# Performance work log

Hardware: AMD Instinct MI355X
Metric: run time of the kernel (lower is better)

The kernel has to match this reference:

```python
import jax, jax.numpy as jnp
import numpy as np

B, N, E, D, L = 64, 128, 2048, 128, 4  # graphs, nodes/graph, edges/graph, channels, gnn layers
T = B * N  # total batched nodes


def setup_inputs() -> dict:
    key = jax.random.key(0)
    ks = jax.random.split(key, 16)
    s = 1.0 / np.sqrt(D)
    sc = 1.0 / np.sqrt(2 * D)
    inp = {
        "x": jax.random.normal(ks[0], (B, N, D), jnp.float32),
        "edges": jax.random.randint(ks[1], (B, 2, E), 0, N, dtype=jnp.int32),
        "Wg": jax.random.normal(ks[2], (L, D, D), jnp.float32) * s,
        "bg": jnp.zeros((L, D), jnp.float32),
        "Wq": jax.random.normal(ks[3], (D, D), jnp.float32) * s,
        "bq": jnp.zeros((D,), jnp.float32),
        "Wk": jax.random.normal(ks[4], (D, D), jnp.float32) * s,
        "bk": jnp.zeros((D,), jnp.float32),
        "Wv": jax.random.normal(ks[5], (D, D), jnp.float32) * s,
        "bv": jnp.zeros((D,), jnp.float32),
        "Wo": jax.random.normal(ks[6], (D, D), jnp.float32) * s,
        "bo": jnp.zeros((D,), jnp.float32),
        "Wc": jax.random.normal(ks[7], (2 * D, D), jnp.float32) * sc,
        "bc": jnp.zeros((D,), jnp.float32),
    }
    return inp


def _batched_edges(edges):
    # offset per-graph edge indices into the flat [T] node space, add self-loops
    off = (jnp.arange(B, dtype=edges.dtype) * N)[:, None]
    src = (edges[:, 0, :] + off).reshape(-1)
    dst = (edges[:, 1, :] + off).reshape(-1)
    loops = jnp.arange(T, dtype=edges.dtype)
    src = jnp.concatenate([src, loops])
    dst = jnp.concatenate([dst, loops])
    return src, dst


def reference(x, edges, Wg, bg, Wq, bq, Wk, bk, Wv, bv, Wo, bo, Wc, bc):
    xf = x.reshape(T, D)  # flat batched node features (torch_geo_batch.x)
    src, dst = _batched_edges(edges)
    # GCN symmetric normalization with self-loops: deg >= 1
    deg = jax.ops.segment_sum(jnp.ones(src.shape, xf.dtype), dst, num_segments=T)
    norm = jax.lax.rsqrt(deg)
    coef = (norm[src] * norm[dst])[:, None]
    # n_layers of GCNConv + tanh
    h = xf
    for l in range(L):
        m = h @ Wg[l]  # [T, D]
        h = jax.ops.segment_sum(m[src] * coef, dst, num_segments=T) + bg[l]
        h = jnp.tanh(h)
    batch_embedding = h.reshape(B, N, D)
    # DoubleHeadedAttention on the ORIGINAL batched input x; both inputs are
    # identical so the two attention heads compute the same tensor.
    q = xf @ Wq + bq
    k = xf @ Wk + bk
    v = xf @ Wv + bv
    attn = jax.nn.softmax(q @ k.T, axis=-1)  # [T, T]
    attended = (attn @ v) @ Wo + bo  # output_layer, == attended_input1 == attended_input2
    combined = jnp.concatenate([attended, attended], axis=-1)  # [T, 2D]
    att_output = combined @ Wc + bc  # combination_layer
    return jnp.concatenate([batch_embedding, att_output.reshape(B, N, D)], axis=-1)
```

## Files before the change

kernel.cpp:

```cpp
#include <hip/hip_runtime.h>
#include <math.h>

#define TT 8192
#define DD 128
#define GB 64
#define GN 128
#define GE 2048

#define WS_W2      (644u<<10)
#define WS_B2      (708u<<10)
#define WS_Q16     (1u<<20)
#define WS_K16     (3u<<20)
#define WS_VT      (5u<<20)
#define WS_OPART   (7u<<20)
#define WS_PM      (23u<<20)
#define WS_PL      ((23u<<20)+(256u<<10))

typedef _Float16 hfrag  __attribute__((ext_vector_type(8)));
typedef _Float16 h4     __attribute__((ext_vector_type(4)));
typedef float    ffrag  __attribute__((ext_vector_type(4)));

#define MFMA16(a,b,c) __builtin_amdgcn_mfma_f32_16x16x32_f16((a),(b),(c),0,0,0)

typedef __attribute__((address_space(1))) unsigned int gu32_t;
typedef __attribute__((address_space(3))) unsigned int lu32_t;
#define GLOAD16(gp, lp) __builtin_amdgcn_global_load_lds((gu32_t*)(const void*)(gp), (lu32_t*)(void*)(lp), 16, 0, 0)

__device__ __forceinline__ int fidx(int r_, int c_) {
  return (((r_>>4)*4 + (c_>>5))*64 + (r_&15) + 16*((c_>>3)&3))*8 + (c_&7);
}

__device__ __forceinline__ float tanh_fast(float x) {
  float e = __expf(2.f*x);
  return 1.f - 2.f/(e+1.f);
}

__global__ __launch_bounds__(512,1) void fused_pre(
    const float* __restrict__ x, const int* __restrict__ edges,
    const float* __restrict__ Wg, const float* __restrict__ bg,
    const float* __restrict__ Wq, const float* __restrict__ bq_,
    const float* __restrict__ Wk, const float* __restrict__ bk_,
    const float* __restrict__ Wv, const float* __restrict__ bv_,
    const float* __restrict__ Wo, const float* __restrict__ bo,
    const float* __restrict__ Wc, const float* __restrict__ bc,
    _Float16* __restrict__ q16, _Float16* __restrict__ k16, _Float16* __restrict__ vT,
    float* __restrict__ W2, float* __restrict__ b2,
    float* __restrict__ out)
{
  __shared__ __align__(16) char Lm[135168];
  const int tid  = threadIdx.x;
  const int bid  = blockIdx.x;

  if (bid < 64) {
    float*    Af  = (float*)Lm;
    _Float16* W16 = (_Float16*)Lm;
    _Float16* m16 = (_Float16*)(Lm + 32768);
    _Float16* h16 = (_Float16*)(Lm + 65536);
    _Float16* A16 = (_Float16*)(Lm + 98304);
    int*      cnt = (int*)(Lm + 131072);
    float*    nrm = (float*)(Lm + 131584);

    const int lane = tid & 63;
    const int w8   = tid >> 6;
    const int l15  = lane & 15;
    const int g    = lane >> 4;
    const int wi   = w8 >> 2;
    const int wj   = w8 & 3;
    const int b    = bid;
    const int* eg  = edges + b*2*GE;

    #pragma unroll
    for (int i=0;i<8;++i) ((float4*)Af)[i*512 + tid] = (float4){0.f,0.f,0.f,0.f};
    if (tid < 128) cnt[tid] = 0;
    __syncthreads();
    #pragma unroll
    for (int i=0;i<4;++i) atomicAdd(&cnt[eg[GE + i*512 + tid]], 1);
    __syncthreads();
    if (tid < 128) nrm[tid] = rsqrtf(1.f + (float)cnt[tid]);
    __syncthreads();
    #pragma unroll
    for (int i=0;i<4;++i){
      int s = eg[i*512 + tid], d = eg[GE + i*512 + tid];
      atomicAdd(&Af[d*128 + s], nrm[s]*nrm[d]);
    }
    __syncthreads();
    if (tid < 128) Af[tid*128 + tid] += nrm[tid]*nrm[tid];
    __syncthreads();
    #pragma unroll
    for (int i=0;i<8;++i){
      int i4 = i*512 + tid;
      float4 v = ((const float4*)Af)[i4];
      int dst = i4>>5, s4 = (i4&31)<<2;
      h4 t; t[0]=(_Float16)v.x; t[1]=(_Float16)v.y; t[2]=(_Float16)v.z; t[3]=(_Float16)v.w;
      *(h4*)&A16[fidx(dst, s4)] = t;
    }
    #pragma unroll
    for (int i=0;i<8;++i){
      int i4 = i*512 + tid;
      int n = i4>>5, k4 = (i4&31)<<2;
      float4 v = *(const float4*)&x[((size_t)b*128 + n)*128 + k4];
      h4 t; t[0]=(_Float16)v.x; t[1]=(_Float16)v.y; t[2]=(_Float16)v.z; t[3]=(_Float16)v.w;
      *(h4*)&h16[fidx(n, k4)] = t;
    }
    __syncthreads();

    for (int l=0; l<4; ++l){
      const float* Wl = Wg + l*DD*DD;
      #pragma unroll
      for (int i=0;i<8;++i){
        int i4 = i*512 + tid;
        int k = i4>>5, i0 = (i4&31)<<2;
        float4 v = *(const float4*)&Wl[k*DD + i0];
        W16[fidx(i0+0,k)] = (_Float16)v.x;
        W16[fidx(i0+1,k)] = (_Float16)v.y;
        W16[fidx(i0+2,k)] = (_Float16)v.z;
        W16[fidx(i0+3,k)] = (_Float16)v.w;
      }
      __syncthreads();

      {
        hfrag bf[2][4];
        #pragma unroll
        for (int jj=0;jj<2;++jj){
          const int jg = wj*2+jj;
          #pragma unroll
          for (int ds=0;ds<4;++ds) bf[jj][ds] = *(const hfrag*)&h16[(jg*4+ds)*512 + lane*8];
        }
        #pragma unroll
        for (int it=0;it<4;++it){
          const int Ri = wi*4+it;
          hfrag af[4];
          #pragma unroll
          for (int ds=0;ds<4;++ds) af[ds] = *(const hfrag*)&W16[(Ri*4+ds)*512 + lane*8];
          #pragma unroll
          for (int jj=0;jj<2;++jj){
            ffrag acc = (ffrag){0.f,0.f,0.f,0.f};
            #pragma unroll
            for (int ds=0;ds<4;++ds) acc = MFMA16(af[ds], bf[jj][ds], acc);
            const int src = (wj*2+jj)*16 + l15;
            const int sds = src>>5, s16 = 16*((src>>3)&3), s7 = src&7;
            #pragma unroll
            for (int r=0;r<4;++r)
              m16[((Ri*4 + sds)*64 + 4*g + r + s16)*8 + s7] = (_Float16)acc[r];
          }
        }
      }
      __syncthreads();

      {
        hfrag bf[2][4];
        float bgv[2];
        #pragma unroll
        for (int jj=0;jj<2;++jj){
          const int jg = wj*2+jj;
          #pragma unroll
          for (int ds=0;ds<4;++ds) bf[jj][ds] = *(const hfrag*)&m16[(jg*4+ds)*512 + lane*8];
          bgv[jj] = bg[l*DD + jg*16 + l15];
        }
        #pragma unroll
        for (int it=0;it<4;++it){
          const int Ri = wi*4+it;
          hfrag af[4];
          #pragma unroll
          for (int ds=0;ds<4;++ds) af[ds] = *(const hfrag*)&A16[(Ri*4+ds)*512 + lane*8];
          #pragma unroll
          for (int jj=0;jj<2;++jj){
            ffrag acc = (ffrag){0.f,0.f,0.f,0.f};
            #pragma unroll
            for (int ds=0;ds<4;++ds) acc = MFMA16(af[ds], bf[jj][ds], acc);
            const int dout = (wj*2+jj)*16 + l15;
            if (l < 3){
              const int dds = dout>>5, d16 = 16*((dout>>3)&3), d7 = dout&7;
              #pragma unroll
              for (int r=0;r<4;++r){
                float v = tanh_fast(acc[r] + bgv[jj]);
                h16[((Ri*4 + dds)*64 + 4*g + r + d16)*8 + d7] = (_Float16)v;
              }
            } else {
              #pragma unroll
              for (int r=0;r<4;++r){
                float v = tanh_fast(acc[r] + bgv[jj]);
                out[((size_t)b*128 + Ri*16 + 4*g + r)*(2*DD) + dout] = v;
              }
            }
          }
        }
      }
      __syncthreads();
    }
  } else if (bid < 256) {
    const int idx  = bid - 64;
    const int mode = idx >> 6;
    const int row0 = (idx & 63) * 128;
    const float* W    = (mode==0) ? Wq : (mode==1) ? Wk : Wv;
    const float* bias = (mode==0) ? bq_ : (mode==1) ? bk_ : bv_;
    float* Xs  = (float*)Lm;
    float* Ws2 = (float*)(Lm + 67584);

    #pragma unroll
    for (int i=0;i<8;++i){
      int i2 = i*512 + tid;
      int r = i2>>5, c4 = (i2&31)<<2;
      *(float4*)&Ws2[r*132+c4] = *(const float4*)&W[r*DD + c4];
      *(float4*)&Xs [r*132+c4] = *(const float4*)&x[(size_t)(row0+r)*DD + c4];
    }
    __syncthreads();

    const int r0 = (tid>>4)*4;
    const int cg = tid&15;
    const int c0 = cg*8;
    float acc[4][8];
    #pragma unroll
    for (int t=0;t<4;++t)
      #pragma unroll
      for (int m=0;m<8;++m) acc[t][m]=0.f;
    for (int kk=0;kk<128;kk+=4){
      float a[4][4];
      #pragma unroll
      for (int t=0;t<4;++t) *(float4*)a[t] = *(float4*)&Xs[(r0+t)*132+kk];
      #pragma unroll
      for (int j=0;j<4;++j){
        float w[8];
        *(float4*)&w[0] = *(float4*)&Ws2[(kk+j)*132+c0];
        *(float4*)&w[4] = *(float4*)&Ws2[(kk+j)*132+c0+4];
        #pragma unroll
        for (int t=0;t<4;++t)
          #pragma unroll
          for (int m=0;m<8;++m) acc[t][m] += a[t][j]*w[m];
      }
    }
    #pragma unroll
    for (int t=0;t<4;++t){
      const int row = row0 + r0 + t;
      float val[8];
      #pragma unroll
      for (int m=0;m<8;++m) val[m] = acc[t][m] + bias[c0+m];
      if (mode == 0) {
        hfrag h;
        #pragma unroll
        for (int m=0;m<8;++m) h[m] = (_Float16)val[m];
        *(hfrag*)&q16[(size_t)row*DD + c0] = h;
      } else if (mode == 1) {
        hfrag h;
        #pragma unroll
        for (int m=0;m<8;++m) h[m] = (_Float16)val[m];
        int R = row>>4, l15r = row&15, dsx = cg>>2, gx = cg&3;
        *(hfrag*)&k16[((size_t)(R*4+dsx)*64 + l15r + 16*gx)*8] = h;
      } else {
        int C = row>>5, kloc = row&31;
        int gx = (kloc&15)>>2;
        int jx = ((kloc>>4)<<2) | (kloc&3);
        #pragma unroll
        for (int m=0;m<8;++m){
          int d = c0+m;
          vT[((size_t)(C*8 + (d>>4))*64 + (d&15) + 16*gx)*8 + jx] = (_Float16)val[m];
        }
      }
    }
  } else {
    const int widx = bid - 256;
    float* Wcs = (float*)Lm;
    #pragma unroll
    for (int i=0;i<32;++i){
      int i2 = i*512 + tid;
      Wcs[i2] = Wc[i2] + Wc[i2 + 16384];
    }
    __syncthreads();
    const int r  = tid>>4;
    const int c0 = (tid&15)*8;
    const int ig = widx*32 + r;
    float acc[8];
    #pragma unroll
    for (int m=0;m<8;++m) acc[m]=0.f;
    for (int k=0;k<128;++k){
      float wo = Wo[ig*DD + k];
      #pragma unroll
      for (int m=0;m<8;++m) acc[m] += wo*Wcs[k*128 + c0 + m];
    }
    #pragma unroll
    for (int m=0;m<8;++m) W2[ig*DD + c0 + m] = acc[m];
    if (widx == 0){
      __syncthreads();
      if (tid < 128){
        float s = bc[tid];
        for (int k=0;k<128;++k) s += bo[k]*Wcs[k*128 + tid];
        b2[tid] = s;
      }
    }
  }
}

__global__ __launch_bounds__(512,2) void k_flash4(
    const _Float16* __restrict__ q16, const _Float16* __restrict__ k16f,
    const _Float16* __restrict__ vTf,
    _Float16* __restrict__ Opart, float* __restrict__ pm, float* __restrict__ pl)
{
  __shared__ _Float16 Kb[2][8192];
  __shared__ _Float16 Vb[2][8192];
  const int tid  = threadIdx.x;
  const int lane = tid & 63;
  const int w8   = tid >> 6;
  const int l15  = lane & 15;
  const int g    = lane >> 4;
  const int qt   = blockIdx.x >> 3;
  const int sp   = blockIdx.x & 7;
  const int q0   = qt*256 + w8*32;

  hfrag qf[2][4];
  #pragma unroll
  for (int qb=0;qb<2;++qb)
    #pragma unroll
    for (int ds=0;ds<4;++ds)
      qf[qb][ds] = *(const hfrag*)&q16[(size_t)(q0+16*qb+l15)*DD + 32*ds + 8*g];

  float mrun[2] = {-1e30f,-1e30f}, lrun[2] = {0.f,0.f};
  ffrag o[2][8];
  #pragma unroll
  for (int qb=0;qb<2;++qb)
    #pragma unroll
    for (int nt=0;nt<8;++nt) o[qb][nt] = (ffrag){0.f,0.f,0.f,0.f};

  const size_t kbase = (size_t)(sp*1024)*DD;
  {
    const _Float16* Ks = k16f + kbase;
    const _Float16* Vs = vTf  + kbase;
    #pragma unroll
    for (int j=0;j<2;++j){
      const int c = w8*2 + j;
      GLOAD16(Ks + c*512 + lane*8, &Kb[0][c*512]);
      GLOAD16(Vs + c*512 + lane*8, &Vb[0][c*512]);
    }
  }
  __syncthreads();

  int cur = 0;
  for (int t=0; t<16; ++t){
    if (t < 15){
      const _Float16* Ks = k16f + kbase + (size_t)(t+1)*64*DD;
      const _Float16* Vs = vTf  + kbase + (size_t)(t+1)*64*DD;
      #pragma unroll
      for (int j=0;j<2;++j){
        const int c = w8*2 + j;
        GLOAD16(Ks + c*512 + lane*8, &Kb[cur^1][c*512]);
        GLOAD16(Vs + c*512 + lane*8, &Vb[cur^1][c*512]);
      }
    }

    ffrag s2[2][4];
    #pragma unroll
    for (int qb=0;qb<2;++qb)
      #pragma unroll
      for (int mt=0;mt<4;++mt) s2[qb][mt] = (ffrag){0.f,0.f,0.f,0.f};
    __builtin_amdgcn_s_setprio(1);
    #pragma unroll
    for (int mt=0;mt<4;++mt)
      #pragma unroll
      for (int ds=0;ds<4;++ds){
        hfrag kf = *(const hfrag*)&Kb[cur][(mt*4+ds)*512 + lane*8];
        s2[0][mt] = MFMA16(kf, qf[0][ds], s2[0][mt]);
        s2[1][mt] = MFMA16(kf, qf[1][ds], s2[1][mt]);
      }
    __builtin_amdgcn_s_setprio(0);

    #pragma unroll
    for (int qb=0;qb<2;++qb){
      float tmax = -1e30f;
      #pragma unroll
      for (int mt=0;mt<4;++mt)
        tmax = fmaxf(tmax, fmaxf(fmaxf(s2[qb][mt][0], s2[qb][mt][1]),
                                 fmaxf(s2[qb][mt][2], s2[qb][mt][3])));
      tmax = fmaxf(tmax, __shfl_xor(tmax,16));
      tmax = fmaxf(tmax, __shfl_xor(tmax,32));
      const float mnew = fmaxf(mrun[qb], tmax);
      float psum = 0.f;
      #pragma unroll
      for (int mt=0;mt<4;++mt)
        #pragma unroll
        for (int r=0;r<4;++r){ float e = __expf(s2[qb][mt][r]-mnew); s2[qb][mt][r]=e; psum += e; }
      psum += __shfl_xor(psum,16);
      psum += __shfl_xor(psum,32);
      if (__any(mnew > mrun[qb])){
        const float sc = __expf(mrun[qb]-mnew);
        lrun[qb] = lrun[qb]*sc + psum;
        mrun[qb] = mnew;
        #pragma unroll
        for (int r=0;r<4;++r){
          const float scr = __shfl(sc, 4*g+r);
          #pragma unroll
          for (int nt=0;nt<8;++nt) o[qb][nt][r] *= scr;
        }
      } else {
        lrun[qb] += psum;
      }
    }

    __builtin_amdgcn_s_setprio(1);
    #pragma unroll
    for (int c2=0;c2<2;++c2){
      hfrag pf0, pf1;
      #pragma unroll
      for (int j=0;j<8;++j){
        pf0[j] = (_Float16)s2[0][2*c2+(j>>2)][j&3];
        pf1[j] = (_Float16)s2[1][2*c2+(j>>2)][j&3];
      }
      #pragma unroll
      for (int nt=0;nt<8;++nt){
        hfrag vf = *(const hfrag*)&Vb[cur][(c2*8+nt)*512 + lane*8];
        o[0][nt] = MFMA16(pf0, vf, o[0][nt]);
        o[1][nt] = MFMA16(pf1, vf, o[1][nt]);
      }
    }
    __builtin_amdgcn_s_setprio(0);

    __syncthreads();
    cur ^= 1;
  }

  #pragma unroll
  for (int qb=0;qb<2;++qb){
    #pragma unroll
    for (int r=0;r<4;++r){
      _Float16* dst = &Opart[((size_t)sp*TT + q0 + 16*qb + 4*g + r)*DD];
      #pragma unroll
      for (int nt=0;nt<8;++nt)
        dst[16*nt + l15] = (_Float16)o[qb][nt][r];
    }
    if (g==0){
      pm[(size_t)sp*TT + q0 + 16*qb + l15] = mrun[qb];
      pl[(size_t)sp*TT + q0 + 16*qb + l15] = lrun[qb];
    }
  }
}

__global__ __launch_bounds__(256) void k_gemm_final(const _Float16* __restrict__ Opart,
                                                    const float* __restrict__ pm, const float* __restrict__ pl,
                                                    const float* __restrict__ W2, const float* __restrict__ b2,
                                                    float* __restrict__ out) {
  __shared__ float As[32*132];
  __shared__ float Ws[128*132];
  int tid = threadIdx.x;
  int row0 = blockIdx.x*32;
  #pragma unroll
  for (int i=0;i<4;i++){
    int idx = i*256+tid;
    int r = idx>>5, c4 = (idx&31)<<2;
    int t = row0 + r;
    float ms[8], ls[8];
    #pragma unroll
    for (int s=0;s<8;++s){ ms[s]=pm[(size_t)s*TT+t]; ls[s]=pl[(size_t)s*TT+t]; }
    float mx = ms[0];
    #pragma unroll
    for (int s=1;s<8;++s) mx = fmaxf(mx, ms[s]);
    float es[8]; float den = 0.f;
    #pragma unroll
    for (int s=0;s<8;++s){ es[s]=__expf(ms[s]-mx); den += ls[s]*es[s]; }
    float4 vv = {0.f,0.f,0.f,0.f};
    #pragma unroll
    for (int s=0;s<8;++s){
      float us = es[s]/den;
      h4 a = *(const h4*)&Opart[((size_t)s*TT + t)*DD + c4];
      vv.x += us*(float)a[0]; vv.y += us*(float)a[1];
      vv.z += us*(float)a[2]; vv.w += us*(float)a[3];
    }
    *(float4*)&As[r*132+c4] = vv;
  }
  #pragma unroll
  for (int i=0;i<16;i++){
    int idx = i*256+tid;
    int r = idx>>5, c4 = (idx&31)<<2;
    *(float4*)&Ws[r*132+c4] = *(const float4*)&W2[r*DD + c4];
  }
  __syncthreads();
  int rg = tid>>4, cg = tid&15;
  int r0 = rg*2, c0 = cg*8;
  float acc[2][8];
  #pragma unroll
  for (int a=0;a<2;a++)
    #pragma unroll
    for (int b=0;b<8;b++) acc[a][b]=0.f;
  for (int kk=0;kk<128;kk+=4){
    float a0[4], a1[4];
    *(float4*)a0 = *(float4*)&As[r0*132+kk];
    *(float4*)a1 = *(float4*)&As[(r0+1)*132+kk];
    #pragma unroll
    for (int j=0;j<4;j++){
      float w[8];
      *(float4*)&w[0] = *(float4*)&Ws[(kk+j)*132+c0];
      *(float4*)&w[4] = *(float4*)&Ws[(kk+j)*132+c0+4];
      #pragma unroll
      for (int m=0;m<8;m++){
        acc[0][m] += a0[j]*w[m];
        acc[1][m] += a1[j]*w[m];
      }
    }
  }
  #pragma unroll
  for (int a=0;a<2;a++){
    float outv[8];
    #pragma unroll
    for (int m=0;m<8;m++) outv[m] = acc[a][m] + b2[c0+m];
    float* dst = &out[(size_t)(row0+r0+a)*(2*DD) + DD + c0];
    *(float4*)&dst[0] = *(float4*)&outv[0];
    *(float4*)&dst[4] = *(float4*)&outv[4];
  }
}

extern "C" void kernel_launch(void* const* d_in, const int* in_sizes, int n_in,
                              void* d_out, int out_size, void* d_ws, size_t ws_size,
                              hipStream_t stream) {
  const float* x  = (const float*)d_in[0];
  const int* edges = (const int*)d_in[1];
  const float* Wg = (const float*)d_in[2];
  const float* bg = (const float*)d_in[3];
  const float* Wq = (const float*)d_in[4];
  const float* bq = (const float*)d_in[5];
  const float* Wk = (const float*)d_in[6];
  const float* bk = (const float*)d_in[7];
  const float* Wv = (const float*)d_in[8];
  const float* bv = (const float*)d_in[9];
  const float* Wo = (const float*)d_in[10];
  const float* bo = (const float*)d_in[11];
  const float* Wc = (const float*)d_in[12];
  const float* bc = (const float*)d_in[13];
  float* out = (float*)d_out;
  char* ws = (char*)d_ws;

  float* W2  = (float*)(ws + WS_W2);
  float* b2  = (float*)(ws + WS_B2);
  float* pm  = (float*)(ws + WS_PM);
  float* pl  = (float*)(ws + WS_PL);
  _Float16* Opart = (_Float16*)(ws + WS_OPART);
  _Float16* q16 = (_Float16*)(ws + WS_Q16);
  _Float16* k16 = (_Float16*)(ws + WS_K16);
  _Float16* vT  = (_Float16*)(ws + WS_VT);

  fused_pre<<<260,512,0,stream>>>(x, edges, Wg, bg, Wq, bq, Wk, bk, Wv, bv,
                                  Wo, bo, Wc, bc, q16, k16, vT, W2, b2, out);
  k_flash4<<<256,512,0,stream>>>(q16, k16, vT, Opart, pm, pl);
  k_gemm_final<<<256,256,0,stream>>>(Opart, pm, pl, W2, b2, out);
}
```

Measured before the change: 109.3 us.

## Precompute fp16 GCN weights in prep kernel and widen flash tiles per wave

A new prep kernel converts the four GCN weight matrices to fp16 in fragment layout and computes the fused Wo·Wc weights, taking that work out of the fused pre-kernel. The GCN blocks then load each layer's weights asynchronously with global-to-LDS loads, overlapped with the aggregation step, instead of converting them in every block. The flash attention kernel now uses 4 waves of 64 queries each instead of 8 waves of 32, so each K/V fragment read from LDS is reused across more query tiles. The trade-offs are one extra kernel launch and higher register pressure, with fewer waves per block in the attention kernel.

Result: slower. 122.2 us (+11.8%).

```diff
diff --git a/kernel.cpp b/kernel.cpp
--- a/kernel.cpp
+++ b/kernel.cpp
@@ -7,6 +7,7 @@
 #define GN 128
 #define GE 2048
 
+#define WS_WG16    0u
 #define WS_W2      (644u<<10)
 #define WS_B2      (708u<<10)
 #define WS_Q16     (1u<<20)
@@ -35,16 +36,66 @@
   return 1.f - 2.f/(e+1.f);
 }
 
+__global__ __launch_bounds__(512) void k_prep(const float* __restrict__ Wg,
+                                              const float* __restrict__ Wo, const float* __restrict__ bo,
+                                              const float* __restrict__ Wc, const float* __restrict__ bc,
+                                              _Float16* __restrict__ wg16,
+                                              float* __restrict__ W2, float* __restrict__ b2) {
+  __shared__ float Wcs[128*128];
+  const int tid = threadIdx.x;
+  const int bid = blockIdx.x;
+  if (bid < 4) {
+    #pragma unroll
+    for (int i=0;i<32;++i){
+      int i2 = i*512 + tid;
+      Wcs[i2] = Wc[i2] + Wc[i2 + 16384];
+    }
+    __syncthreads();
+    const int r  = tid>>4;
+    const int c0 = (tid&15)*8;
+    const int ig = bid*32 + r;
+    float acc[8];
+    #pragma unroll
+    for (int m=0;m<8;++m) acc[m]=0.f;
+    for (int k=0;k<128;++k){
+      float wo = Wo[ig*DD + k];
+      #pragma unroll
+      for (int m=0;m<8;++m) acc[m] += wo*Wcs[k*128 + c0 + m];
+    }
+    #pragma unroll
+    for (int m=0;m<8;++m) W2[ig*DD + c0 + m] = acc[m];
+    if (bid == 0){
+      __syncthreads();
+      if (tid < 128){
+        float s = bc[tid];
+        for (int k=0;k<128;++k) s += bo[k]*Wcs[k*128 + tid];
+        b2[tid] = s;
+      }
+    }
+  } else {
+    const int l = bid - 4;
+    const float* Wl = Wg + l*DD*DD;
+    _Float16* dst = wg16 + l*16384;
+    #pragma unroll
+    for (int i=0;i<8;++i){
+      int i4 = i*512 + tid;
+      int k = i4>>5, i0 = (i4&31)<<2;
+      float4 v = *(const float4*)&Wl[k*DD + i0];
+      dst[fidx(i0+0,k)] = (_Float16)v.x;
+      dst[fidx(i0+1,k)] = (_Float16)v.y;
+      dst[fidx(i0+2,k)] = (_Float16)v.z;
+      dst[fidx(i0+3,k)] = (_Float16)v.w;
+    }
+  }
+}
+
 __global__ __launch_bounds__(512,1) void fused_pre(
     const float* __restrict__ x, const int* __restrict__ edges,
-    const float* __restrict__ Wg, const float* __restrict__ bg,
+    const _Float16* __restrict__ wg16, const float* __restrict__ bg,
     const float* __restrict__ Wq, const float* __restrict__ bq_,
     const float* __restrict__ Wk, const float* __restrict__ bk_,
     const float* __restrict__ Wv, const float* __restrict__ bv_,
-    const float* __restrict__ Wo, const float* __restrict__ bo,
-    const float* __restrict__ Wc, const float* __restrict__ bc,
     _Float16* __restrict__ q16, _Float16* __restrict__ k16, _Float16* __restrict__ vT,
-    float* __restrict__ W2, float* __restrict__ b2,
     float* __restrict__ out)
 {
   __shared__ __align__(16) char Lm[135168];
@@ -52,13 +103,13 @@
   const int bid  = blockIdx.x;
 
   if (bid < 64) {
-    float*    Af  = (float*)Lm;
-    _Float16* W16 = (_Float16*)Lm;
-    _Float16* m16 = (_Float16*)(Lm + 32768);
-    _Float16* h16 = (_Float16*)(Lm + 65536);
-    _Float16* A16 = (_Float16*)(Lm + 98304);
-    int*      cnt = (int*)(Lm + 131072);
-    float*    nrm = (float*)(Lm + 131584);
+    float*    Af   = (float*)Lm;
+    _Float16* W16f = (_Float16*)Lm;
+    _Float16* m16  = (_Float16*)(Lm + 32768);
+    _Float16* h16  = (_Float16*)(Lm + 65536);
+    _Float16* A16  = (_Float16*)(Lm + 98304);
+    int*      cnt  = (int*)(Lm + 131072);
+    float*    nrm  = (float*)(Lm + 131584);
 
     const int lane = tid & 63;
     const int w8   = tid >> 6;
@@ -103,21 +154,15 @@
       *(h4*)&h16[fidx(n, k4)] = t;
     }
     __syncthreads();
+    #pragma unroll
+    for (int i=0;i<4;++i){
+      const int c = i*8 + w8;
+      GLOAD16(wg16 + c*512 + lane*8, &W16f[c*512]);
+    }
+    asm volatile("s_waitcnt vmcnt(0)" ::: "memory");
+    __syncthreads();
 
     for (int l=0; l<4; ++l){
-      const float* Wl = Wg + l*DD*DD;
-      #pragma unroll
-      for (int i=0;i<8;++i){
-        int i4 = i*512 + tid;
-        int k = i4>>5, i0 = (i4&31)<<2;
-        float4 v = *(const float4*)&Wl[k*DD + i0];
-        W16[fidx(i0+0,k)] = (_Float16)v.x;
-        W16[fidx(i0+1,k)] = (_Float16)v.y;
-        W16[fidx(i0+2,k)] = (_Float16)v.z;
-        W16[fidx(i0+3,k)] = (_Float16)v.w;
-      }
-      __syncthreads();
-
       {
         hfrag bf[2][4];
         #pragma unroll
@@ -131,7 +176,7 @@
           const int Ri = wi*4+it;
           hfrag af[4];
           #pragma unroll
-          for (int ds=0;ds<4;++ds) af[ds] = *(const hfrag*)&W16[(Ri*4+ds)*512 + lane*8];
+          for (int ds=0;ds<4;++ds) af[ds] = *(const hfrag*)&W16f[(Ri*4+ds)*512 + lane*8];
           #pragma unroll
           for (int jj=0;jj<2;++jj){
             ffrag acc = (ffrag){0.f,0.f,0.f,0.f};
@@ -146,7 +191,13 @@
         }
       }
       __syncthreads();
-
+      if (l < 3){
+        #pragma unroll
+        for (int i=0;i<4;++i){
+          const int c = i*8 + w8;
+          GLOAD16(wg16 + (l+1)*16384 + c*512 + lane*8, &W16f[c*512]);
+        }
+      }
       {
         hfrag bf[2][4];
         float bgv[2];
@@ -188,7 +239,7 @@
       }
       __syncthreads();
     }
-  } else if (bid < 256) {
+  } else {
     const int idx  = bid - 64;
     const int mode = idx >> 6;
     const int row0 = (idx & 63) * 128;
@@ -257,40 +308,10 @@
         }
       }
     }
-  } else {
-    const int widx = bid - 256;
-    float* Wcs = (float*)Lm;
-    #pragma unroll
-    for (int i=0;i<32;++i){
-      int i2 = i*512 + tid;
-      Wcs[i2] = Wc[i2] + Wc[i2 + 16384];
-    }
-    __syncthreads();
-    const int r  = tid>>4;
-    const int c0 = (tid&15)*8;
-    const int ig = widx*32 + r;
-    float acc[8];
-    #pragma unroll
-    for (int m=0;m<8;++m) acc[m]=0.f;
-    for (int k=0;k<128;++k){
-      float wo = Wo[ig*DD + k];
-      #pragma unroll
-      for (int m=0;m<8;++m) acc[m] += wo*Wcs[k*128 + c0 + m];
-    }
-    #pragma unroll
-    for (int m=0;m<8;++m) W2[ig*DD + c0 + m] = acc[m];
-    if (widx == 0){
-      __syncthreads();
-      if (tid < 128){
-        float s = bc[tid];
-        for (int k=0;k<128;++k) s += bo[k]*Wcs[k*128 + tid];
-        b2[tid] = s;
-      }
-    }
-  }
-}
-
-__global__ __launch_bounds__(512,2) void k_flash4(
+  }
+}
+
+__global__ __launch_bounds__(256,1) void k_flash5(
     const _Float16* __restrict__ q16, const _Float16* __restrict__ k16f,
     const _Float16* __restrict__ vTf,
     _Float16* __restrict__ Opart, float* __restrict__ pm, float* __restrict__ pl)
@@ -299,24 +320,24 @@
   __shared__ _Float16 Vb[2][8192];
   const int tid  = threadIdx.x;
   const int lane = tid & 63;
-  const int w8   = tid >> 6;
+  const int w4   = tid >> 6;
   const int l15  = lane & 15;
   const int g    = lane >> 4;
   const int qt   = blockIdx.x >> 3;
   const int sp   = blockIdx.x & 7;
-  const int q0   = qt*256 + w8*32;
-
-  hfrag qf[2][4];
-  #pragma unroll
-  for (int qb=0;qb<2;++qb)
+  const int q0   = qt*256 + w4*64;
+
+  hfrag qf[4][4];
+  #pragma unroll
+  for (int qb=0;qb<4;++qb)
     #pragma unroll
     for (int ds=0;ds<4;++ds)
       qf[qb][ds] = *(const hfrag*)&q16[(size_t)(q0+16*qb+l15)*DD + 32*ds + 8*g];
 
-  float mrun[2] = {-1e30f,-1e30f}, lrun[2] = {0.f,0.f};
-  ffrag o[2][8];
-  #pragma unroll
-  for (int qb=0;qb<2;++qb)
+  float mrun[4] = {-1e30f,-1e30f,-1e30f,-1e30f}, lrun[4] = {0.f,0.f,0.f,0.f};
+  ffrag o[4][8];
+  #pragma unroll
+  for (int qb=0;qb<4;++qb)
     #pragma unroll
     for (int nt=0;nt<8;++nt) o[qb][nt] = (ffrag){0.f,0.f,0.f,0.f};
 
@@ -325,8 +346,8 @@
     const _Float16* Ks = k16f + kbase;
     const _Float16* Vs = vTf  + kbase;
     #pragma unroll
-    for (int j=0;j<2;++j){
-      const int c = w8*2 + j;
+    for (int j=0;j<4;++j){
+      const int c = w4*4 + j;
       GLOAD16(Ks + c*512 + lane*8, &Kb[0][c*512]);
       GLOAD16(Vs + c*512 + lane*8, &Vb[0][c*512]);
     }
@@ -339,16 +360,16 @@
       const _Float16* Ks = k16f + kbase + (size_t)(t+1)*64*DD;
       const _Float16* Vs = vTf  + kbase + (size_t)(t+1)*64*DD;
       #pragma unroll
-      for (int j=0;j<2;++j){
-        const int c = w8*2 + j;
+      for (int j=0;j<4;++j){
+        const int c = w4*4 + j;
         GLOAD16(Ks + c*512 + lane*8, &Kb[cur^1][c*512]);
         GLOAD16(Vs + c*512 + lane*8, &Vb[cur^1][c*512]);
       }
     }
 
-    ffrag s2[2][4];
-    #pragma unroll
-    for (int qb=0;qb<2;++qb)
+    ffrag s2[4][4];
+    #pragma unroll
+    for (int qb=0;qb<4;++qb)
       #pragma unroll
       for (int mt=0;mt<4;++mt) s2[qb][mt] = (ffrag){0.f,0.f,0.f,0.f};
     __builtin_amdgcn_s_setprio(1);
@@ -357,13 +378,14 @@
       #pragma unroll
       for (int ds=0;ds<4;++ds){
         hfrag kf = *(const hfrag*)&Kb[cur][(mt*4+ds)*512 + lane*8];
-        s2[0][mt] = MFMA16(kf, qf[0][ds], s2[0][mt]);
-        s2[1][mt] = MFMA16(kf, qf[1][ds], s2[1][mt]);
+        #pragma unroll
+        for (int qb=0;qb<4;++qb)
+          s2[qb][mt] = MFMA16(kf, qf[qb][ds], s2[qb][mt]);
       }
     __builtin_amdgcn_s_setprio(0);
 
     #pragma unroll
-    for (int qb=0;qb<2;++qb){
+    for (int qb=0;qb<4;++qb){
       float tmax = -1e30f;
       #pragma unroll
       for (int mt=0;mt<4;++mt)
@@ -397,17 +419,17 @@
     __builtin_amdgcn_s_setprio(1);
     #pragma unroll
     for (int c2=0;c2<2;++c2){
-      hfrag pf0, pf1;
-      #pragma unroll
-      for (int j=0;j<8;++j){
-        pf0[j] = (_Float16)s2[0][2*c2+(j>>2)][j&3];
-        pf1[j] = (_Float16)s2[1][2*c2+(j>>2)][j&3];
-      }
+      hfrag pf[4];
+      #pragma unroll
+      for (int qb=0;qb<4;++qb)
+        #pragma unroll
+        for (int j=0;j<8;++j) pf[qb][j] = (_Float16)s2[qb][2*c2+(j>>2)][j&3];
       #pragma unroll
       for (int nt=0;nt<8;++nt){
         hfrag vf = *(const hfrag*)&Vb[cur][(c2*8+nt)*512 + lane*8];
-        o[0][nt] = MFMA16(pf0, vf, o[0][nt]);
-        o[1][nt] = MFMA16(pf1, vf, o[1][nt]);
+        #pragma unroll
+        for (int qb=0;qb<4;++qb)
+          o[qb][nt] = MFMA16(pf[qb], vf, o[qb][nt]);
       }
     }
     __builtin_amdgcn_s_setprio(0);
@@ -417,7 +439,7 @@
   }
 
   #pragma unroll
-  for (int qb=0;qb<2;++qb){
+  for (int qb=0;qb<4;++qb){
     #pragma unroll
     for (int r=0;r<4;++r){
       _Float16* dst = &Opart[((size_t)sp*TT + q0 + 16*qb + 4*g + r)*DD];
@@ -525,6 +547,7 @@
   float* out = (float*)d_out;
   char* ws = (char*)d_ws;
 
+  _Float16* wg16 = (_Float16*)(ws + WS_WG16);
   float* W2  = (float*)(ws + WS_W2);
   float* b2  = (float*)(ws + WS_B2);
   float* pm  = (float*)(ws + WS_PM);
@@ -534,8 +557,9 @@
   _Float16* k16 = (_Float16*)(ws + WS_K16);
   _Float16* vT  = (_Float16*)(ws + WS_VT);
 
-  fused_pre<<<260,512,0,stream>>>(x, edges, Wg, bg, Wq, bq, Wk, bk, Wv, bv,
-                                  Wo, bo, Wc, bc, q16, k16, vT, W2, b2, out);
-  k_flash4<<<256,512,0,stream>>>(q16, k16, vT, Opart, pm, pl);
+  k_prep<<<8,512,0,stream>>>(Wg, Wo, bo, Wc, bc, wg16, W2, b2);
+  fused_pre<<<256,512,0,stream>>>(x, edges, wg16, bg, Wq, bq, Wk, bk, Wv, bv,
+                                  q16, k16, vT, out);
+  k_flash5<<<256,256,0,stream>>>(q16, k16, vT, Opart, pm, pl);
   k_gemm_final<<<256,256,0,stream>>>(Opart, pm, pl, W2, b2, out);
 }
```
